# Performance work log

Hardware: AMD Instinct MI355X
Metric: run time of the kernel (lower is better)

Reference implementation:

```python
import jax, jax.numpy as jnp
import numpy as np

RES = 256
DEC = 8
NUM_MEAS = RES * RES // DEC  # 8192
BATCH = 4


def _bilinear_gather(img, coords):
    """grid_sample-style bilinear interpolation (align_corners=True, zero padding).
    img: [B, C, H, W]; coords: [M, 2] with (x, y) in pixel-centered units [-res/2, res/2].
    Returns [B, C, M]."""
    B, C, H, W = img.shape
    # normalize to [-1, 1] then map to pixel index space (align_corners=True)
    gx = (coords[:, 0] / (W / 2) + 1.0) * 0.5 * (W - 1)
    gy = (coords[:, 1] / (H / 2) + 1.0) * 0.5 * (H - 1)
    x0 = jnp.floor(gx)
    y0 = jnp.floor(gy)
    wx1 = gx - x0
    wx0 = 1.0 - wx1
    wy1 = gy - y0
    wy0 = 1.0 - wy1
    x0i = x0.astype(jnp.int32)
    y0i = y0.astype(jnp.int32)

    def tap(xi, yi, w):
        valid = ((xi >= 0) & (xi < W) & (yi >= 0) & (yi < H)).astype(img.dtype)
        xc = jnp.clip(xi, 0, W - 1)
        yc = jnp.clip(yi, 0, H - 1)
        v = img[:, :, yc, xc]  # [B, C, M] advanced-index gather
        return v * (w * valid)[None, None, :]

    return (tap(x0i, y0i, wx0 * wy0) + tap(x0i + 1, y0i, wx1 * wy0)
            + tap(x0i, y0i + 1, wx0 * wy1) + tap(x0i + 1, y0i + 1, wx1 * wy1))


def _nufft_adjoint(s, coords, N):
    """Exact adjoint non-uniform DFT (the math the gridding NUFFT approximates).
    s: [B, M] complex samples at k-space locations coords [M, 2] (pixel units, centered).
    out[b, y, x] = sum_m s[b,m] * exp(2j*pi*(kx_m*(x-N/2) + ky_m*(y-N/2))/N)."""
    n = jnp.arange(N, dtype=jnp.float32) - N / 2  # centered image coords
    two_pi = jnp.float32(2.0 * np.pi)
    Ex = jnp.exp(1j * (two_pi * coords[:, 0:1] * n[None, :] / N)).astype(jnp.complex64)  # [M, N]
    Ey = jnp.exp(1j * (two_pi * coords[:, 1:2] * n[None, :] / N)).astype(jnp.complex64)  # [M, N]
    t = s[:, :, None] * Ey[None, :, :]          # [B, M, H]
    return jnp.einsum('bmy,mx->byx', t, Ex)     # [B, H, W] complex64


def setup_inputs() -> dict:
    key = jax.random.key(0)
    k1, k2 = jax.random.split(key)
    inp = jax.random.normal(k1, (BATCH, 1, RES, RES, 2), dtype=jnp.float32)
    # gaussian trajectory init: randn * res / 6 (learnable parameter)
    x = jax.random.normal(k2, (NUM_MEAS, 2), dtype=jnp.float32) * (RES / 6.0)
    return {"input": inp, "x": x}


def reference(input, x):
    # [B,1,H,W,2] -> [B,2,H,W] (real/imag as channels)
    img = jnp.transpose(input, (0, 1, 4, 2, 3))[:, 0]
    B, C, H, W = img.shape
    sub_ksp = _bilinear_gather(img, x)                      # [B, 2, M]
    s = (sub_ksp[:, 0] + 1j * sub_ksp[:, 1]).astype(jnp.complex64)  # [B, M]
    out_c = _nufft_adjoint(s, x, H)                          # [B, H, W]
    out = jnp.stack([out_c.real, out_c.imag], axis=-1)       # [B, H, W, 2]
    return out[:, None]                                      # [B, 1, H, W, 2]
```

## Files before the change

### kernel.cpp

```cpp
#include <hip/hip_runtime.h>
#include <hip/hip_bf16.h>
#include <stdint.h>
#include <math.h>

#define RES     256
#define M_MEAS  8192
#define KDIM    8192
#define ROWSC   2048
#define NCOLS   288
#define SINOFF  144
#define SPLIT   16
#define KCHUNK  512
#define BM      128
#define BN      144
#define BK      64
#define NT      (KCHUNK / BK)
#define TWO_PI  6.28318530717958647692f

typedef __attribute__((ext_vector_type(8))) __bf16 bf16x8;
typedef __attribute__((ext_vector_type(8))) unsigned short u16x8;
typedef __attribute__((ext_vector_type(4))) float f32x4;
typedef __attribute__((ext_vector_type(2))) float f32x2;

#define OFF_SRE 0
#define OFF_SIM 131072
#define OFF_KY  262144
#define OFF_B   294912
#define OFF_C   5013504

__device__ __forceinline__ unsigned short f2bf(float f) {
    unsigned u = __float_as_uint(f);
    u += 0x7FFFu + ((u >> 16) & 1u);
    return (unsigned short)(u >> 16);
}

__device__ __forceinline__ float bf2f(unsigned short v) {
    unsigned u = ((unsigned)v) << 16;
    return __uint_as_float(u);
}

__device__ __forceinline__ void lds_load16(const void* g, void* l) {
    __builtin_amdgcn_global_load_lds(
        (const __attribute__((address_space(1))) uint32_t*)(uintptr_t)g,
        (__attribute__((address_space(3))) uint32_t*)(uint32_t)(uintptr_t)l,
        16, 0, 0);
}

__global__ __launch_bounds__(256) void k_prep(const float* __restrict__ in,
                                              const float* __restrict__ xs,
                                              float* __restrict__ sRe,
                                              float* __restrict__ sIm,
                                              float* __restrict__ kyc,
                                              unsigned short* __restrict__ Bt) {
    int blk = blockIdx.x;
    if (blk < 128) {
        int t = blk * 256 + threadIdx.x;
        int b = t >> 13, m = t & (M_MEAS - 1);
        float kx = xs[2 * m + 0], ky = xs[2 * m + 1];
        if (t < M_MEAS) kyc[t] = xs[2 * t + 1];
        float gx = (kx * (1.0f / 128.0f) + 1.0f) * 0.5f * 255.0f;
        float gy = (ky * (1.0f / 128.0f) + 1.0f) * 0.5f * 255.0f;
        float fx0 = floorf(gx), fy0 = floorf(gy);
        float wx1 = gx - fx0, wx0 = 1.0f - wx1;
        float wy1 = gy - fy0, wy0 = 1.0f - wy1;
        int x0 = (int)fx0, y0 = (int)fy0;
        float re = 0.0f, im = 0.0f;
#pragma unroll
        for (int dy = 0; dy < 2; ++dy) {
#pragma unroll
            for (int dx = 0; dx < 2; ++dx) {
                int xi = x0 + dx, yi = y0 + dy;
                bool v = (xi >= 0) && (xi < RES) && (yi >= 0) && (yi < RES);
                int xc = min(max(xi, 0), RES - 1);
                int yc = min(max(yi, 0), RES - 1);
                float w = (dx ? wx1 : wx0) * (dy ? wy1 : wy0) * (v ? 1.0f : 0.0f);
                const float* p = in + ((((size_t)b * RES + yc) * RES + xc) * 2);
                re += p[0] * w;
                im += p[1] * w;
            }
        }
        sRe[b * M_MEAS + m] = re;
        sIm[b * M_MEAS + m] = im;
    } else {
        int t = (blk - 128) * 256 + threadIdx.x;
        int cidx = t >> 10;
        int m0 = (t & 1023) * 8;
        bool isCos = cidx < SINOFF;
        int u = isCos ? cidx : (cidx - SINOFF);
        u16x8 v;
        if (u > 128) {
            v = (u16x8){0, 0, 0, 0, 0, 0, 0, 0};
        } else {
            float nn = (float)u;
#pragma unroll
            for (int j = 0; j < 8; ++j) {
                float kx = xs[2 * (m0 + j) + 0];
                float ur = kx * nn * (1.0f / 256.0f);
                ur -= rintf(ur);
                float th = ur * TWO_PI;
                v[j] = f2bf(isCos ? __cosf(th) : __sinf(th));
            }
        }
        *(u16x8*)(Bt + (size_t)cidx * KDIM + m0) = v;
    }
}

__global__ __launch_bounds__(256, 2) void k_gemm(const float* __restrict__ sReG,
                                                 const float* __restrict__ sImG,
                                                 const float* __restrict__ kyG,
                                                 const unsigned short* __restrict__ Bt,
                                                 unsigned short* __restrict__ Cp) {
    __shared__ __align__(16) unsigned short As[2][BM * BK];
    __shared__ __align__(16) unsigned short Bs[2][BN * BK];
    __shared__ __align__(16) float sbuf[3 * KCHUNK];

    int bid = blockIdx.x;
    int tc = bid & 1, rest = bid >> 1;
    int tr = rest & 15, split = rest >> 4;
    int col0 = tc * BN;
    int kbase = split * KCHUNK;
    int yhalf = tr & 1, isIm = (tr >> 1) & 1, batch = tr >> 2;
    int tid = threadIdx.x;
    int w = tid >> 6, l = tid & 63;
    int lr = l & 15, lu = l >> 4;

    f32x4 acc[2][9] = {};

#define STAGE_B(buf, kt)                                                          \
    do {                                                                          \
        _Pragma("unroll")                                                         \
        for (int q = 0; q < 5; ++q) {                                             \
            int U = q * 256 + tid; if (U >= 1152) U -= 1152;                      \
            int r = U >> 3, u = U & 7;                                            \
            lds_load16(Bt + (size_t)(col0 + r) * KDIM + kbase + (kt) * BK         \
                          + ((u ^ (r & 7)) * 8),                                  \
                       &Bs[buf][U * 8]);                                          \
        }                                                                         \
    } while (0)

#define GEN_A(buf, kt)                                                            \
    do {                                                                          \
        int p = tid & 31, g = tid >> 5;                                           \
        int mi = (kt) * BK + p * 2;                                               \
        float2 kyp = *(const float2*)&sbuf[mi];                                   \
        float2 srp = *(const float2*)&sbuf[KCHUNK + mi];                          \
        float2 sip = *(const float2*)&sbuf[2 * KCHUNK + mi];                      \
        float n0 = (float)(yhalf * 128 + g * 16 - 128);                           \
        float c0, s0, c1, s1, cs0, ss0, cs1, ss1;                                 \
        { float u = kyp.x * n0 * (1.0f/256.0f); u -= rintf(u);                    \
          s0 = __sinf(u * TWO_PI); c0 = __cosf(u * TWO_PI); }                     \
        { float u = kyp.x * (1.0f/256.0f); u -= rintf(u);                         \
          ss0 = __sinf(u * TWO_PI); cs0 = __cosf(u * TWO_PI); }                   \
        { float u = kyp.y * n0 * (1.0f/256.0f); u -= rintf(u);                    \
          s1 = __sinf(u * TWO_PI); c1 = __cosf(u * TWO_PI); }                     \
        { float u = kyp.y * (1.0f/256.0f); u -= rintf(u);                         \
          ss1 = __sinf(u * TWO_PI); cs1 = __cosf(u * TWO_PI); }                   \
        _Pragma("unroll")                                                         \
        for (int j = 0; j < 16; ++j) {                                            \
            int r = g * 16 + j;                                                   \
            float v0 = isIm ? fmaf(srp.x, s0, sip.x * c0)                         \
                            : fmaf(srp.x, c0, -(sip.x * s0));                     \
            float v1 = isIm ? fmaf(srp.y, s1, sip.y * c1)                         \
                            : fmaf(srp.y, c1, -(sip.y * s1));                     \
            unsigned pk = (unsigned)f2bf(v0) | ((unsigned)f2bf(v1) << 16);        \
            *(unsigned*)&As[buf][r * 64 + (((p >> 2) ^ (r & 7)) * 8) + (p & 3) * 2] = pk; \
            float nc0 = fmaf(c0, cs0, -(s0 * ss0));                               \
            float ns0 = fmaf(s0, cs0,  (c0 * ss0));                               \
            c0 = nc0; s0 = ns0;                                                   \
            float nc1 = fmaf(c1, cs1, -(s1 * ss1));                               \
            float ns1 = fmaf(s1, cs1,  (c1 * ss1));                               \
            c1 = nc1; s1 = ns1;                                                   \
        }                                                                         \
    } while (0)

#pragma unroll
    for (int q = 0; q < 2; ++q) {
        int V = q * 256 + tid; if (V >= 384) V -= 384;
        int rg = V >> 7, idx = V & 127;
        const float* s = (rg == 0) ? kyG
                       : (rg == 1) ? (sReG + (size_t)batch * M_MEAS)
                                   : (sImG + (size_t)batch * M_MEAS);
        lds_load16(s + kbase + idx * 4, &sbuf[V * 4]);
    }
    STAGE_B(0, 0);
    asm volatile("s_waitcnt vmcnt(5)" ::: "memory");
    __builtin_amdgcn_s_barrier();
    GEN_A(0, 0);
    asm volatile("s_waitcnt vmcnt(0) lgkmcnt(0)" ::: "memory");
    __builtin_amdgcn_sched_barrier(0);
    __builtin_amdgcn_s_barrier();

    for (int t = 0; t < NT; ++t) {
        int cur = t & 1;
        if (t < NT - 1) {
            STAGE_B(cur ^ 1, t + 1);
            GEN_A(cur ^ 1, t + 1);
        }

        bf16x8 af[2][2], bfr[2][9];
#pragma unroll
        for (int ks = 0; ks < 2; ++ks) {
            int uu = ks * 4 + lu;
#pragma unroll
            for (int i = 0; i < 2; ++i) {
                int r = w * 32 + i * 16 + lr;
                af[ks][i] = *(const bf16x8*)&As[cur][r * 64 + ((uu ^ (r & 7)) * 8)];
            }
#pragma unroll
            for (int j = 0; j < 9; ++j) {
                int r = j * 16 + lr;
                bfr[ks][j] = *(const bf16x8*)&Bs[cur][r * 64 + ((uu ^ (r & 7)) * 8)];
            }
        }
        asm volatile("s_waitcnt lgkmcnt(0)" ::: "memory");
        __builtin_amdgcn_sched_barrier(0);
        __builtin_amdgcn_s_setprio(1);
#pragma unroll
        for (int ks = 0; ks < 2; ++ks)
#pragma unroll
            for (int i = 0; i < 2; ++i)
#pragma unroll
                for (int j = 0; j < 9; ++j)
                    acc[i][j] = __builtin_amdgcn_mfma_f32_16x16x32_bf16(af[ks][i], bfr[ks][j], acc[i][j], 0, 0, 0);
        __builtin_amdgcn_s_setprio(0);
        asm volatile("s_waitcnt vmcnt(0)" ::: "memory");
        __builtin_amdgcn_sched_barrier(0);
        __builtin_amdgcn_s_barrier();
    }
#undef STAGE_B
#undef GEN_A

    unsigned short* Cb = Cp + (size_t)split * ROWSC * NCOLS;
#pragma unroll
    for (int i = 0; i < 2; ++i) {
#pragma unroll
        for (int j = 0; j < 9; ++j) {
            int colg = col0 + j * 16 + lr;
#pragma unroll
            for (int v = 0; v < 4; ++v) {
                int rowg = tr * BM + w * 32 + i * 16 + lu * 4 + v;
                Cb[(size_t)rowg * NCOLS + colg] = f2bf(acc[i][j][v]);
            }
        }
    }
}

__global__ __launch_bounds__(256) void k_combine(const unsigned short* __restrict__ Cp,
                                                 float* __restrict__ out) {
    __shared__ float part[4 * 68 * 9];
    int blk = blockIdx.x;
    int b = blk >> 8, y = blk & 255;
    int tid = threadIdx.x;
    int q = tid >> 6, un = tid & 63;

    size_t rRe = ((size_t)b * 512 + y) * NCOLS;
    size_t rIm = rRe + (size_t)256 * NCOLS;

#pragma unroll
    for (int rep = 0; rep < 2; ++rep) {
        int unit = un + rep * 64;
        if (rep == 1 && un >= 4) break;
        int seg = unit / 17, uidx = unit - seg * 17;
        size_t base = ((seg & 2) ? rIm : rRe) + ((seg & 1) ? SINOFF : 0) + uidx * 8;
        float a[8] = {};
#pragma unroll
        for (int s2 = 0; s2 < 4; ++s2) {
            const unsigned short* Cb = Cp + (size_t)(q * 4 + s2) * ROWSC * NCOLS;
            u16x8 v = *(const u16x8*)(Cb + base);
#pragma unroll
            for (int k = 0; k < 8; ++k) a[k] += bf2f(v[k]);
        }
#pragma unroll
        for (int k = 0; k < 8; ++k) part[(q * 68 + unit) * 9 + k] = a[k];
    }
    __syncthreads();

    if (tid < 68) {
#pragma unroll
        for (int k = 0; k < 8; ++k) {
            float s = part[(0 * 68 + tid) * 9 + k] + part[(1 * 68 + tid) * 9 + k]
                    + part[(2 * 68 + tid) * 9 + k] + part[(3 * 68 + tid) * 9 + k];
            part[tid * 9 + k] = s;
        }
    }
    __syncthreads();

    int x = tid;
    int n = x - 128;
    int u = (n < 0) ? -n : n;
    float sg = (n < 0) ? -1.0f : 1.0f;
    int ui = u >> 3, uk = u & 7;
    float cr = part[(0 * 17 + ui) * 9 + uk];
    float sr = part[(17 + ui) * 9 + uk];
    float ci = part[(34 + ui) * 9 + uk];
    float si = part[(51 + ui) * 9 + uk];
    float re = cr - sg * si;
    float im = sg * sr + ci;
    ((f32x2*)out)[(size_t)(b * 256 + y) * 256 + x] = (f32x2){re, im};
}

extern "C" void kernel_launch(void* const* d_in, const int* in_sizes, int n_in,
                              void* d_out, int out_size, void* d_ws, size_t ws_size,
                              hipStream_t stream) {
    const float* in = (const float*)d_in[0];
    const float* xs = (const float*)d_in[1];
    float* out = (float*)d_out;
    char* ws = (char*)d_ws;

    float* sRe = (float*)(ws + OFF_SRE);
    float* sIm = (float*)(ws + OFF_SIM);
    float* kyc = (float*)(ws + OFF_KY);
    unsigned short* Bt = (unsigned short*)(ws + OFF_B);
    unsigned short* Cp = (unsigned short*)(ws + OFF_C);

    k_prep   <<<128 + 1152, 256, 0, stream>>>(in, xs, sRe, sIm, kyc, Bt);
    k_gemm   <<<512,        256, 0, stream>>>(sRe, sIm, kyc, Bt, Cp);
    k_combine<<<1024,       256, 0, stream>>>(Cp, out);
}
```

Measured before the change: 40.60 us.

## Fuse prep into GEMM: generate Ex tiles on the fly and gather in-block

Removes the k_prep kernel. Each GEMM block now performs its own bilinear gather for its K-chunk and generates the cos/sin Ex operand directly into LDS with a rotation recurrence, instead of staging a precomputed Bt matrix from global memory. This drops one launch and the global write and read of the Bt and sample buffers. In exchange the gather is repeated across blocks (each block recomputes samples for its split), B-tile generation adds ALU and transcendental work to the GEMM main loop, and the recurrence can lose accuracy at high frequencies.

```diff
diff --git a/kernel.cpp b/kernel.cpp
--- a/kernel.cpp
+++ b/kernel.cpp
@@ -22,97 +22,29 @@
 typedef __attribute__((ext_vector_type(4))) float f32x4;
 typedef __attribute__((ext_vector_type(2))) float f32x2;
 
-#define OFF_SRE 0
-#define OFF_SIM 131072
-#define OFF_KY  262144
-#define OFF_B   294912
-#define OFF_C   5013504
-
-__device__ __forceinline__ unsigned short f2bf(float f) {
-    unsigned u = __float_as_uint(f);
-    u += 0x7FFFu + ((u >> 16) & 1u);
-    return (unsigned short)(u >> 16);
-}
 
 __device__ __forceinline__ float bf2f(unsigned short v) {
     unsigned u = ((unsigned)v) << 16;
     return __uint_as_float(u);
 }
 
-__device__ __forceinline__ void lds_load16(const void* g, void* l) {
-    __builtin_amdgcn_global_load_lds(
-        (const __attribute__((address_space(1))) uint32_t*)(uintptr_t)g,
-        (__attribute__((address_space(3))) uint32_t*)(uint32_t)(uintptr_t)l,
-        16, 0, 0);
-}
-
-__global__ __launch_bounds__(256) void k_prep(const float* __restrict__ in,
-                                              const float* __restrict__ xs,
-                                              float* __restrict__ sRe,
-                                              float* __restrict__ sIm,
-                                              float* __restrict__ kyc,
-                                              unsigned short* __restrict__ Bt) {
-    int blk = blockIdx.x;
-    if (blk < 128) {
-        int t = blk * 256 + threadIdx.x;
-        int b = t >> 13, m = t & (M_MEAS - 1);
-        float kx = xs[2 * m + 0], ky = xs[2 * m + 1];
-        if (t < M_MEAS) kyc[t] = xs[2 * t + 1];
-        float gx = (kx * (1.0f / 128.0f) + 1.0f) * 0.5f * 255.0f;
-        float gy = (ky * (1.0f / 128.0f) + 1.0f) * 0.5f * 255.0f;
-        float fx0 = floorf(gx), fy0 = floorf(gy);
-        float wx1 = gx - fx0, wx0 = 1.0f - wx1;
-        float wy1 = gy - fy0, wy0 = 1.0f - wy1;
-        int x0 = (int)fx0, y0 = (int)fy0;
-        float re = 0.0f, im = 0.0f;
-#pragma unroll
-        for (int dy = 0; dy < 2; ++dy) {
-#pragma unroll
-            for (int dx = 0; dx < 2; ++dx) {
-                int xi = x0 + dx, yi = y0 + dy;
-                bool v = (xi >= 0) && (xi < RES) && (yi >= 0) && (yi < RES);
-                int xc = min(max(xi, 0), RES - 1);
-                int yc = min(max(yi, 0), RES - 1);
-                float w = (dx ? wx1 : wx0) * (dy ? wy1 : wy0) * (v ? 1.0f : 0.0f);
-                const float* p = in + ((((size_t)b * RES + yc) * RES + xc) * 2);
-                re += p[0] * w;
-                im += p[1] * w;
-            }
-        }
-        sRe[b * M_MEAS + m] = re;
-        sIm[b * M_MEAS + m] = im;
-    } else {
-        int t = (blk - 128) * 256 + threadIdx.x;
-        int cidx = t >> 10;
-        int m0 = (t & 1023) * 8;
-        bool isCos = cidx < SINOFF;
-        int u = isCos ? cidx : (cidx - SINOFF);
-        u16x8 v;
-        if (u > 128) {
-            v = (u16x8){0, 0, 0, 0, 0, 0, 0, 0};
-        } else {
-            float nn = (float)u;
-#pragma unroll
-            for (int j = 0; j < 8; ++j) {
-                float kx = xs[2 * (m0 + j) + 0];
-                float ur = kx * nn * (1.0f / 256.0f);
-                ur -= rintf(ur);
-                float th = ur * TWO_PI;
-                v[j] = f2bf(isCos ? __cosf(th) : __sinf(th));
-            }
-        }
-        *(u16x8*)(Bt + (size_t)cidx * KDIM + m0) = v;
-    }
-}
-
-__global__ __launch_bounds__(256, 2) void k_gemm(const float* __restrict__ sReG,
-                                                 const float* __restrict__ sImG,
-                                                 const float* __restrict__ kyG,
-                                                 const unsigned short* __restrict__ Bt,
+__device__ __forceinline__ unsigned pack2bf(float a, float b) {
+    unsigned short ha = __bfloat16_as_ushort(__float2bfloat16(a));
+    unsigned short hb = __bfloat16_as_ushort(__float2bfloat16(b));
+    return (unsigned)ha | ((unsigned)hb << 16);
+}
+
+#define SB_KX 0
+#define SB_KY 512
+#define SB_RE 1024
+#define SB_IM 1536
+
+__global__ __launch_bounds__(256, 2) void k_gemm(const float* __restrict__ in,
+                                                 const float* __restrict__ xs,
                                                  unsigned short* __restrict__ Cp) {
     __shared__ __align__(16) unsigned short As[2][BM * BK];
     __shared__ __align__(16) unsigned short Bs[2][BN * BK];
-    __shared__ __align__(16) float sbuf[3 * KCHUNK];
+    __shared__ __align__(16) float sbuf[4 * 512];
 
     int bid = blockIdx.x;
     int tc = bid & 1, rest = bid >> 1;
@@ -126,25 +58,53 @@
 
     f32x4 acc[2][9] = {};
 
-#define STAGE_B(buf, kt)                                                          \
-    do {                                                                          \
-        _Pragma("unroll")                                                         \
-        for (int q = 0; q < 5; ++q) {                                             \
-            int U = q * 256 + tid; if (U >= 1152) U -= 1152;                      \
-            int r = U >> 3, u = U & 7;                                            \
-            lds_load16(Bt + (size_t)(col0 + r) * KDIM + kbase + (kt) * BK         \
-                          + ((u ^ (r & 7)) * 8),                                  \
-                       &Bs[buf][U * 8]);                                          \
-        }                                                                         \
-    } while (0)
+    {
+        int i0 = tid * 2;
+        int m = kbase + i0;
+        f32x4 xv = *(const f32x4*)(xs + 2 * m);
+        sbuf[SB_KX + i0]     = xv.x;
+        sbuf[SB_KY + i0]     = xv.y;
+        sbuf[SB_KX + i0 + 1] = xv.z;
+        sbuf[SB_KY + i0 + 1] = xv.w;
+        const float* img = in + (size_t)batch * RES * RES * 2;
+#pragma unroll
+        for (int e = 0; e < 2; ++e) {
+            float kx = e ? xv.z : xv.x;
+            float ky = e ? xv.w : xv.y;
+            float gx = (kx * (1.0f / 128.0f) + 1.0f) * 0.5f * 255.0f;
+            float gy = (ky * (1.0f / 128.0f) + 1.0f) * 0.5f * 255.0f;
+            float fx0 = floorf(gx), fy0 = floorf(gy);
+            float wx1 = gx - fx0, wx0 = 1.0f - wx1;
+            float wy1 = gy - fy0, wy0 = 1.0f - wy1;
+            int x0 = (int)fx0, y0 = (int)fy0;
+            float re = 0.0f, im = 0.0f;
+#pragma unroll
+            for (int dy = 0; dy < 2; ++dy) {
+#pragma unroll
+                for (int dx = 0; dx < 2; ++dx) {
+                    int xi = x0 + dx, yi = y0 + dy;
+                    bool v = (xi >= 0) && (xi < RES) && (yi >= 0) && (yi < RES);
+                    int xc = min(max(xi, 0), RES - 1);
+                    int yc = min(max(yi, 0), RES - 1);
+                    float wt = (dx ? wx1 : wx0) * (dy ? wy1 : wy0) * (v ? 1.0f : 0.0f);
+                    const float* p = img + (((size_t)yc * RES + xc) * 2);
+                    re += p[0] * wt;
+                    im += p[1] * wt;
+                }
+            }
+            sbuf[SB_RE + i0 + e] = re;
+            sbuf[SB_IM + i0 + e] = im;
+        }
+    }
+    __syncthreads();
 
 #define GEN_A(buf, kt)                                                            \
     do {                                                                          \
         int p = tid & 31, g = tid >> 5;                                           \
         int mi = (kt) * BK + p * 2;                                               \
-        float2 kyp = *(const float2*)&sbuf[mi];                                   \
-        float2 srp = *(const float2*)&sbuf[KCHUNK + mi];                          \
-        float2 sip = *(const float2*)&sbuf[2 * KCHUNK + mi];                      \
+        float2 kyp = *(const float2*)&sbuf[SB_KY + mi];                           \
+        float2 srp = *(const float2*)&sbuf[SB_RE + mi];                           \
+        float2 sip = *(const float2*)&sbuf[SB_IM + mi];                           \
         float n0 = (float)(yhalf * 128 + g * 16 - 128);                           \
         float c0, s0, c1, s1, cs0, ss0, cs1, ss1;                                 \
         { float u = kyp.x * n0 * (1.0f/256.0f); u -= rintf(u);                    \
@@ -162,8 +122,8 @@
                             : fmaf(srp.x, c0, -(sip.x * s0));                     \
             float v1 = isIm ? fmaf(srp.y, s1, sip.y * c1)                         \
                             : fmaf(srp.y, c1, -(sip.y * s1));                     \
-            unsigned pk = (unsigned)f2bf(v0) | ((unsigned)f2bf(v1) << 16);        \
-            *(unsigned*)&As[buf][r * 64 + (((p >> 2) ^ (r & 7)) * 8) + (p & 3) * 2] = pk; \
+            *(unsigned*)&As[buf][r * 64 + (((p >> 2) ^ (r & 7)) * 8) + (p & 3) * 2] \
+                = pack2bf(v0, v1);                                                \
             float nc0 = fmaf(c0, cs0, -(s0 * ss0));                               \
             float ns0 = fmaf(s0, cs0,  (c0 * ss0));                               \
             c0 = nc0; s0 = ns0;                                                   \
@@ -173,27 +133,46 @@
         }                                                                         \
     } while (0)
 
-#pragma unroll
-    for (int q = 0; q < 2; ++q) {
-        int V = q * 256 + tid; if (V >= 384) V -= 384;
-        int rg = V >> 7, idx = V & 127;
-        const float* s = (rg == 0) ? kyG
-                       : (rg == 1) ? (sReG + (size_t)batch * M_MEAS)
-                                   : (sImG + (size_t)batch * M_MEAS);
-        lds_load16(s + kbase + idx * 4, &sbuf[V * 4]);
-    }
-    STAGE_B(0, 0);
-    asm volatile("s_waitcnt vmcnt(5)" ::: "memory");
-    __builtin_amdgcn_s_barrier();
+#define GEN_B(buf, kt)                                                            \
+    do {                                                                          \
+        int p = tid & 31, g = tid >> 5;                                           \
+        int mi = (kt) * BK + p * 2;                                               \
+        float2 kxp = *(const float2*)&sbuf[SB_KX + mi];                           \
+        float r0 = (float)(g * 18);                                               \
+        float c0, s0, c1, s1, cs0, ss0, cs1, ss1;                                 \
+        { float u = kxp.x * r0 * (1.0f/256.0f); u -= rintf(u);                    \
+          s0 = __sinf(u * TWO_PI); c0 = __cosf(u * TWO_PI); }                     \
+        { float u = kxp.x * (1.0f/256.0f); u -= rintf(u);                         \
+          ss0 = __sinf(u * TWO_PI); cs0 = __cosf(u * TWO_PI); }                   \
+        { float u = kxp.y * r0 * (1.0f/256.0f); u -= rintf(u);                    \
+          s1 = __sinf(u * TWO_PI); c1 = __cosf(u * TWO_PI); }                     \
+        { float u = kxp.y * (1.0f/256.0f); u -= rintf(u);                         \
+          ss1 = __sinf(u * TWO_PI); cs1 = __cosf(u * TWO_PI); }                   \
+        _Pragma("unroll")                                                         \
+        for (int j = 0; j < 18; ++j) {                                            \
+            int r = g * 18 + j;                                                   \
+            float live = (r <= 128) ? 1.0f : 0.0f;                                \
+            float v0 = (tc ? s0 : c0) * live;                                     \
+            float v1 = (tc ? s1 : c1) * live;                                     \
+            *(unsigned*)&Bs[buf][r * 64 + (((p >> 2) ^ (r & 7)) * 8) + (p & 3) * 2] \
+                = pack2bf(v0, v1);                                                \
+            float nc0 = fmaf(c0, cs0, -(s0 * ss0));                               \
+            float ns0 = fmaf(s0, cs0,  (c0 * ss0));                               \
+            c0 = nc0; s0 = ns0;                                                   \
+            float nc1 = fmaf(c1, cs1, -(s1 * ss1));                               \
+            float ns1 = fmaf(s1, cs1,  (c1 * ss1));                               \
+            c1 = nc1; s1 = ns1;                                                   \
+        }                                                                         \
+    } while (0)
+
+    GEN_B(0, 0);
     GEN_A(0, 0);
-    asm volatile("s_waitcnt vmcnt(0) lgkmcnt(0)" ::: "memory");
-    __builtin_amdgcn_sched_barrier(0);
-    __builtin_amdgcn_s_barrier();
+    __syncthreads();
 
     for (int t = 0; t < NT; ++t) {
         int cur = t & 1;
         if (t < NT - 1) {
-            STAGE_B(cur ^ 1, t + 1);
+            GEN_B(cur ^ 1, t + 1);
             GEN_A(cur ^ 1, t + 1);
         }
 
@@ -223,12 +202,11 @@
                 for (int j = 0; j < 9; ++j)
                     acc[i][j] = __builtin_amdgcn_mfma_f32_16x16x32_bf16(af[ks][i], bfr[ks][j], acc[i][j], 0, 0, 0);
         __builtin_amdgcn_s_setprio(0);
-        asm volatile("s_waitcnt vmcnt(0)" ::: "memory");
         __builtin_amdgcn_sched_barrier(0);
         __builtin_amdgcn_s_barrier();
     }
-#undef STAGE_B
 #undef GEN_A
+#undef GEN_B
 
     unsigned short* Cb = Cp + (size_t)split * ROWSC * NCOLS;
 #pragma unroll
@@ -239,7 +217,8 @@
 #pragma unroll
             for (int v = 0; v < 4; ++v) {
                 int rowg = tr * BM + w * 32 + i * 16 + lu * 4 + v;
-                Cb[(size_t)rowg * NCOLS + colg] = f2bf(acc[i][j][v]);
+                Cb[(size_t)rowg * NCOLS + colg] =
+                    __bfloat16_as_ushort(__float2bfloat16(acc[i][j][v]));
             }
         }
     }
@@ -305,15 +284,8 @@
     const float* in = (const float*)d_in[0];
     const float* xs = (const float*)d_in[1];
     float* out = (float*)d_out;
-    char* ws = (char*)d_ws;
-
-    float* sRe = (float*)(ws + OFF_SRE);
-    float* sIm = (float*)(ws + OFF_SIM);
-    float* kyc = (float*)(ws + OFF_KY);
-    unsigned short* Bt = (unsigned short*)(ws + OFF_B);
-    unsigned short* Cp = (unsigned short*)(ws + OFF_C);
-
-    k_prep   <<<128 + 1152, 256, 0, stream>>>(in, xs, sRe, sIm, kyc, Bt);
-    k_gemm   <<<512,        256, 0, stream>>>(sRe, sIm, kyc, Bt, Cp);
-    k_combine<<<1024,       256, 0, stream>>>(Cp, out);
-}
+    unsigned short* Cp = (unsigned short*)d_ws;
+
+    k_gemm   <<<512,  256, 0, stream>>>(in, xs, Cp);
+    k_combine<<<1024, 256, 0, stream>>>(Cp, out);
+}
```

New measurement: 45.50 us. +12.1%, slower.
